# Performance work log

Hardware: AMD Instinct MI355X
Metric: run time of the kernel (lower is better)

The kernel has to match this reference:

```python
import jax, jax.numpy as jnp
import numpy as np

N_NODES = 100000
N_EDGES = 1600000
IN_D = 128
OUT_D = 128


def setup_inputs() -> dict:
    key = jax.random.key(0)
    ks = jax.random.split(key, 10)
    scale = 1.0 / np.sqrt(IN_D)
    inp = {
        "x": jax.random.normal(ks[0], (N_NODES, IN_D), dtype=jnp.float32),
        "edge_idx": jax.random.randint(ks[1], (2, N_EDGES), 0, N_NODES, dtype=jnp.int32),
        "W1": jax.random.normal(ks[2], (OUT_D, IN_D), dtype=jnp.float32) * scale,
        "b1": jax.random.normal(ks[3], (OUT_D,), dtype=jnp.float32) * scale,
        "W2": jax.random.normal(ks[4], (OUT_D, IN_D), dtype=jnp.float32) * scale,
        "b2": jax.random.normal(ks[5], (OUT_D,), dtype=jnp.float32) * scale,
        "W3": jax.random.normal(ks[6], (OUT_D, IN_D), dtype=jnp.float32) * scale,
        "b3": jax.random.normal(ks[7], (OUT_D,), dtype=jnp.float32) * scale,
        "W4": jax.random.normal(ks[8], (OUT_D, IN_D), dtype=jnp.float32) * scale,
        "b4": jax.random.normal(ks[9], (OUT_D,), dtype=jnp.float32) * scale,
    }
    return inp


def _message_passing(y, src, dst, num_nodes, add_self=True):
    # original: if add_self: x = x + x  (doubles features)
    if add_self:
        y = y + y
    # gather messages from source nodes, scatter-add into target nodes
    return jax.ops.segment_sum(y[src], dst, num_segments=num_nodes)


def reference(x, edge_idx, W1, b1, W2, b2, W3, b3, W4, b4):
    num_nodes = x.shape[0]
    src, dst = edge_idx[0], edge_idx[1]
    x1 = x @ W1.T + b1
    x2 = _message_passing(x @ W2.T + b2, src, dst, num_nodes)
    x3 = _message_passing(x @ W3.T + b3, src, dst, num_nodes)
    x4 = _message_passing(x @ W4.T + b4, src, dst, num_nodes)
    return jax.nn.sigmoid(x3 + x4) * x2 + x1
```

## Files before the change

kernel.cpp:

```cpp
#include <hip/hip_runtime.h>

__device__ __forceinline__ float bf2f(unsigned short u) {
    union { unsigned int i; float f; } v;
    v.i = ((unsigned int)u) << 16;
    return v.f;
}
__device__ __forceinline__ unsigned short f2bf(float f) {
    union { float f; unsigned int i; } v;
    v.f = f;
    unsigned int x = v.i;
    return (unsigned short)((x + 0x7fffu + ((x >> 16) & 1u)) >> 16);
}

typedef short bf16x8 __attribute__((ext_vector_type(8)));
typedef float f32x4 __attribute__((ext_vector_type(4)));

#define BSHIFT 9
#define BRANGE 512

__global__ void prep_kernel(const float* __restrict__ x,
                            const float* __restrict__ W1, const float* __restrict__ W2,
                            const float* __restrict__ W3, const float* __restrict__ W4,
                            unsigned short* __restrict__ xb, unsigned short* __restrict__ Wb,
                            int* __restrict__ deg, int* __restrict__ bcnt, int M, int nx4)
{
    int i = blockIdx.x * 256 + threadIdx.x;
    if (i < nx4) {
        float4 v = ((const float4*)x)[i];
        unsigned lo = (unsigned)f2bf(v.x) | ((unsigned)f2bf(v.y) << 16);
        unsigned hi = (unsigned)f2bf(v.z) | ((unsigned)f2bf(v.w) << 16);
        uint2 p; p.x = lo; p.y = hi;
        *(uint2*)(xb + (size_t)i * 4) = p;
    }
    if (deg && i < M) deg[i] = 0;
    if (bcnt && i < 256) bcnt[i] = 0;
    if (i < 16384) {
        Wb[i]         = f2bf(W1[i]);
        Wb[16384 + i] = f2bf(W2[i]);
        Wb[32768 + i] = f2bf(W3[i] + W4[i]);
    }
}

__global__ __launch_bounds__(512) void bucket_hist_kernel(
    const int* __restrict__ dst, int* __restrict__ bcnt, int ne, int nb)
{
    __shared__ int h[256];
    int t = threadIdx.x;
    if (t < 256) h[t] = 0;
    __syncthreads();
    for (int i = blockIdx.x * 512 + t; i < ne; i += gridDim.x * 512)
        atomicAdd(&h[dst[i] >> BSHIFT], 1);
    __syncthreads();
    if (t < nb) {
        int c = h[t];
        if (c) atomicAdd(&bcnt[t], c);
    }
}

__global__ __launch_bounds__(256) void bucket_scan_kernel(
    const int* __restrict__ bcnt, int* __restrict__ boff, int* __restrict__ gcur, int nb)
{
    __shared__ int sh[256];
    int t = threadIdx.x;
    int v = (t < nb) ? bcnt[t] : 0;
    sh[t] = v;
    __syncthreads();
    int acc = v;
    for (int off = 1; off < 256; off <<= 1) {
        int y = (t >= off) ? sh[t - off] : 0;
        __syncthreads();
        acc += y;
        sh[t] = acc;
        __syncthreads();
    }
    if (t < nb) {
        boff[t + 1] = acc;
        gcur[t] = acc - v;
    }
    if (t == 0) boff[0] = 0;
}

__global__ __launch_bounds__(512) void bucketize_kernel(
    const int* __restrict__ src, const int* __restrict__ dst,
    int* __restrict__ gcur, int2* __restrict__ bucketed, int ne, int chunk)
{
    __shared__ int cnt[256];
    __shared__ int sbase[256];
    const int t = threadIdx.x;
    const int e0 = blockIdx.x * chunk;
    const int e1 = (e0 + chunk < ne) ? e0 + chunk : ne;

    if (t < 256) cnt[t] = 0;
    __syncthreads();
    for (int e = e0 + t; e < e1; e += 512)
        atomicAdd(&cnt[dst[e] >> BSHIFT], 1);
    __syncthreads();
    if (t < 256) {
        int c = cnt[t];
        sbase[t] = c ? atomicAdd(&gcur[t], c) : 0;
        cnt[t] = 0;
    }
    __syncthreads();
    for (int e = e0 + t; e < e1; e += 512) {
        int d = dst[e];
        int b = d >> BSHIFT;
        int loc = atomicAdd(&cnt[b], 1);
        int2 v; v.x = src[e]; v.y = d;
        bucketed[sbase[b] + loc] = v;
    }
}

__global__ __launch_bounds__(512) void bucket_count_kernel(
    const int2* __restrict__ bucketed, const int* __restrict__ boff,
    int* __restrict__ deg, int M)
{
    __shared__ int cnt[BRANGE];
    const int t = threadIdx.x;
    const int b = blockIdx.x;
    cnt[t] = 0;
    __syncthreads();
    const int lo = boff[b], hi = boff[b + 1];
    for (int i = lo + t; i < hi; i += 512)
        atomicAdd(&cnt[bucketed[i].y & (BRANGE - 1)], 1);
    __syncthreads();
    int node = (b << BSHIFT) + t;
    if (node < M) deg[node] = cnt[t];
}

__global__ __launch_bounds__(512) void bucket_fill_kernel(
    const int2* __restrict__ bucketed, const int* __restrict__ boff,
    const int* __restrict__ offs, int* __restrict__ csr, int M)
{
    __shared__ int cur[BRANGE];
    const int t = threadIdx.x;
    const int b = blockIdx.x;
    int node = (b << BSHIFT) + t;
    cur[t] = (node < M) ? offs[node] : 0;
    __syncthreads();
    const int lo = boff[b], hi = boff[b + 1];
    for (int i = lo + t; i < hi; i += 512) {
        int2 e = bucketed[i];
        int p = atomicAdd(&cur[e.y & (BRANGE - 1)], 1);
        csr[p] = e.x;
    }
}

__global__ void hist_kernel(const int* __restrict__ dst, int* __restrict__ deg, int ne) {
    int e = blockIdx.x * blockDim.x + threadIdx.x;
    if (e < ne) atomicAdd(&deg[dst[e]], 1);
}

__global__ __launch_bounds__(1024) void scan_local_kernel(
    const int* __restrict__ deg, int* __restrict__ offs, int* __restrict__ bsum, int n)
{
    __shared__ int sh[1024];
    int t = threadIdx.x;
    int i = blockIdx.x * 1024 + t;
    int v = (i < n) ? deg[i] : 0;
    sh[t] = v;
    __syncthreads();
    int acc = v;
    for (int off = 1; off < 1024; off <<= 1) {
        int y = (t >= off) ? sh[t - off] : 0;
        __syncthreads();
        acc += y;
        sh[t] = acc;
        __syncthreads();
    }
    if (i < n) offs[i] = acc - v;
    if (t == 1023) bsum[blockIdx.x] = acc;
}

__global__ __launch_bounds__(128) void scan_totals_kernel(
    int* __restrict__ bsum, int* __restrict__ offs, int nb, int n)
{
    __shared__ int sh[128];
    int t = threadIdx.x;
    int v = (t < nb) ? bsum[t] : 0;
    sh[t] = v;
    __syncthreads();
    int acc = v;
    for (int off = 1; off < 128; off <<= 1) {
        int y = (t >= off) ? sh[t - off] : 0;
        __syncthreads();
        acc += y;
        sh[t] = acc;
        __syncthreads();
    }
    if (t < nb) bsum[t] = acc - v;
    if (t == 127) offs[n] = acc;
}

__global__ __launch_bounds__(1024) void scan_finalize_kernel(
    int* __restrict__ offs, const int* __restrict__ bsum, int* __restrict__ cursor, int n)
{
    int i = blockIdx.x * 1024 + threadIdx.x;
    if (i < n) {
        int o = offs[i] + bsum[i >> 10];
        offs[i] = o;
        if (cursor) cursor[i] = o;
    }
}

__global__ __launch_bounds__(256) void fill_csr_ranged_kernel(
    const int* __restrict__ src, const int* __restrict__ dst,
    int* __restrict__ cursor, int* __restrict__ csr, int ne, int rangeSize)
{
    const int r = blockIdx.x & 7;
    const int cb = blockIdx.x >> 3;
    const int nchunk = gridDim.x >> 3;
    const unsigned lo = (unsigned)(r * rangeSize);
    for (int e = cb * 256 + threadIdx.x; e < ne; e += nchunk * 256) {
        int d = dst[e];
        int s = src[e];
        if ((unsigned)(d - lo) < (unsigned)rangeSize) {
            int pos = atomicAdd(&cursor[d], 1);
            csr[pos] = s;
        }
    }
}

template<bool BF16SRC>
__global__ __launch_bounds__(256) void gather_kernel(
    const void* __restrict__ xsrc, const int* __restrict__ offs,
    const int* __restrict__ csr, unsigned short* __restrict__ gb, int M)
{
    const int wave = threadIdx.x >> 6;
    const int lane = threadIdx.x & 63;
    const int node = blockIdx.x * 4 + wave;
    if (node >= M) return;
    const int e0 = offs[node];
    const int e1 = offs[node + 1];

    float s0 = 0.f, s1 = 0.f, t0 = 0.f, t1 = 0.f;
    for (int e = e0; e < e1; e += 8) {
        int id[8];
        float m[8];
#pragma unroll
        for (int j = 0; j < 8; ++j) {
            int ee = e + j;
            bool ok = ee < e1;
            id[j] = csr[ok ? ee : e1 - 1];
            m[j] = ok ? 1.f : 0.f;
        }
#pragma unroll
        for (int j = 0; j < 8; ++j) {
            float lo, hi;
            if (BF16SRC) {
                unsigned v = *(const unsigned*)((const unsigned short*)xsrc +
                                                (size_t)id[j] * 128 + lane * 2);
                lo = bf2f((unsigned short)(v & 0xffffu));
                hi = bf2f((unsigned short)(v >> 16));
            } else {
                float2 v = *(const float2*)((const float*)xsrc +
                                            (size_t)id[j] * 128 + lane * 2);
                lo = v.x;
                hi = v.y;
            }
            if (j & 1) { t0 += m[j] * lo; t1 += m[j] * hi; }
            else       { s0 += m[j] * lo; s1 += m[j] * hi; }
        }
    }
    unsigned pk = (unsigned)f2bf(s0 + t0) | ((unsigned)f2bf(s1 + t1) << 16);
    *(unsigned*)(gb + (size_t)node * 128 + lane * 2) = pk;
}

template<bool XBF16>
__global__ __launch_bounds__(256) void gemm_kernel(
    const void* __restrict__ xsrc, const unsigned short* __restrict__ gb,
    const int* __restrict__ deg, const unsigned short* __restrict__ Wb,
    const float* __restrict__ B1, const float* __restrict__ B2,
    const float* __restrict__ B3, const float* __restrict__ B4,
    float* __restrict__ out, int M)
{
    __shared__ unsigned short x_lds[32 * 136];
    __shared__ unsigned short g_lds[32 * 136];

    const int t = threadIdx.x;
    const int wave = t >> 6;
    const int lane = t & 63;
    const int ln = lane & 15;
    const int quad = lane >> 4;
    const int row0 = blockIdx.x * 32;

    if (XBF16) {
        const unsigned short* xb = (const unsigned short*)xsrc;
#pragma unroll
        for (int i = 0; i < 2; ++i) {
            int c = i * 256 + t;
            int row = c >> 4;
            int koff = (c & 15) * 8;
            int grow = row0 + row;
            if (grow > M - 1) grow = M - 1;
            *(uint4*)&x_lds[row * 136 + koff] =
                *(const uint4*)(xb + (size_t)grow * 128 + koff);
        }
    } else {
        const float* xf = (const float*)xsrc;
#pragma unroll
        for (int i = 0; i < 4; ++i) {
            int c = i * 256 + t;
            int row = c >> 5;
            int koff = (c & 31) * 4;
            int grow = row0 + row;
            if (grow > M - 1) grow = M - 1;
            float4 v = *(const float4*)(xf + (size_t)grow * 128 + koff);
            unsigned p0 = (unsigned)f2bf(v.x) | ((unsigned)f2bf(v.y) << 16);
            unsigned p1 = (unsigned)f2bf(v.z) | ((unsigned)f2bf(v.w) << 16);
            *(unsigned*)&x_lds[row * 136 + koff]     = p0;
            *(unsigned*)&x_lds[row * 136 + koff + 2] = p1;
        }
    }
#pragma unroll
    for (int i = 0; i < 2; ++i) {
        int c = i * 256 + t;
        int row = c >> 4;
        int koff = (c & 15) * 8;
        int grow = row0 + row;
        if (grow > M - 1) grow = M - 1;
        *(uint4*)&g_lds[row * 136 + koff] =
            *(const uint4*)(gb + (size_t)grow * 128 + koff);
    }
    __syncthreads();

    f32x4 acc[3][2][2];
#pragma unroll
    for (int p = 0; p < 3; ++p)
#pragma unroll
        for (int rt = 0; rt < 2; ++rt)
#pragma unroll
            for (int c = 0; c < 2; ++c) {
                acc[p][rt][c][0] = 0.f; acc[p][rt][c][1] = 0.f;
                acc[p][rt][c][2] = 0.f; acc[p][rt][c][3] = 0.f;
            }

#pragma unroll
    for (int kk = 0; kk < 4; ++kk) {
        bf16x8 ax[2], ag[2];
#pragma unroll
        for (int rt = 0; rt < 2; ++rt) {
            ax[rt] = *(const bf16x8*)&x_lds[(rt * 16 + ln) * 136 + kk * 32 + quad * 8];
            ag[rt] = *(const bf16x8*)&g_lds[(rt * 16 + ln) * 136 + kk * 32 + quad * 8];
        }
#pragma unroll
        for (int p = 0; p < 3; ++p) {
#pragma unroll
            for (int c = 0; c < 2; ++c) {
                int col = wave * 32 + c * 16 + ln;
                bf16x8 bw = *(const bf16x8*)(Wb + (size_t)p * 16384 +
                                             (size_t)col * 128 + kk * 32 + quad * 8);
#pragma unroll
                for (int rt = 0; rt < 2; ++rt) {
                    acc[p][rt][c] = __builtin_amdgcn_mfma_f32_16x16x32_bf16(
                        (p == 0) ? ax[rt] : ag[rt], bw, acc[p][rt][c], 0, 0, 0);
                }
            }
        }
    }

#pragma unroll
    for (int rt = 0; rt < 2; ++rt) {
#pragma unroll
        for (int i = 0; i < 4; ++i) {
            int row = row0 + rt * 16 + quad * 4 + i;
            if (row < M) {
                float dg = (float)deg[row];
#pragma unroll
                for (int c = 0; c < 2; ++c) {
                    int col = wave * 32 + c * 16 + ln;
                    float p1 = acc[0][rt][c][i] + B1[col];
                    float h2 = 2.f * (acc[1][rt][c][i] + dg * B2[col]);
                    float z  = 2.f * (acc[2][rt][c][i] + dg * (B3[col] + B4[col]));
                    float g = 1.f / (1.f + __expf(-z));
                    out[(size_t)row * 128 + col] = g * h2 + p1;
                }
            }
        }
    }
}

extern "C" void kernel_launch(void* const* d_in, const int* in_sizes, int n_in,
                              void* d_out, int out_size, void* d_ws, size_t ws_size,
                              hipStream_t stream) {
    const float* x  = (const float*)d_in[0];
    const int* eidx = (const int*)d_in[1];
    const float* W1 = (const float*)d_in[2];
    const float* B1 = (const float*)d_in[3];
    const float* W2 = (const float*)d_in[4];
    const float* B2 = (const float*)d_in[5];
    const float* W3 = (const float*)d_in[6];
    const float* B3 = (const float*)d_in[7];
    const float* W4 = (const float*)d_in[8];
    const float* B4 = (const float*)d_in[9];
    float* out      = (float*)d_out;

    const int M  = in_sizes[0] / 128;
    const int NE = in_sizes[1] / 2;
    const int* src = eidx;
    const int* dst = eidx + NE;

    const int NB = (M + BRANGE - 1) >> BSHIFT;

    auto pad = [](size_t b) { return (b + 127) & ~(size_t)127; };
    const size_t xb_bytes  = pad((size_t)M * 128 * 2);
    const size_t gb_bytes  = pad((size_t)M * 128 * 2);
    const size_t wb_bytes  = pad((size_t)3 * 16384 * 2);
    const size_t deg_bytes = pad((size_t)M * 4);
    const size_t off_bytes = pad((size_t)(M + 1) * 4);
    const size_t csr_bytes = pad((size_t)NE * 4);
    const size_t bkt_bytes = pad((size_t)NE * 8);

    const size_t need_full = xb_bytes + gb_bytes + wb_bytes + deg_bytes + off_bytes +
                             1024 + csr_bytes + bkt_bytes + 4 * 1024;
    const bool full = (NB <= 256) && ws_size >= need_full + 1024;

    char* ws = (char*)d_ws;
    size_t off = 0;
    auto take = [&](size_t bytes) -> char* {
        char* p = ws + off;
        off = (off + bytes + 127) & ~(size_t)127;
        return p;
    };

    const int nbScan = (M + 1023) / 1024;

    if (full) {
        unsigned short* xb = (unsigned short*)take(xb_bytes);
        unsigned short* gb = (unsigned short*)take(gb_bytes);
        unsigned short* Wb = (unsigned short*)take(wb_bytes);
        int* deg   = (int*)take((size_t)M * 4);
        int* offs  = (int*)take((size_t)(M + 1) * 4);
        int* bsum  = (int*)take(256 * 4);
        int* csr   = (int*)take((size_t)NE * 4);
        int2* bkt  = (int2*)take((size_t)NE * 8);
        int* bcnt  = (int*)take(256 * 4);
        int* boff  = (int*)take(257 * 4);
        int* gcur  = (int*)take(256 * 4);

        const int nx4 = M * 128 / 4;
        const int chunk = (NE + 255) / 256;

        prep_kernel<<<(M * 32 + 255) / 256, 256, 0, stream>>>(
            x, W1, W2, W3, W4, xb, Wb, deg, bcnt, M, nx4);
        bucket_hist_kernel<<<256, 512, 0, stream>>>(dst, bcnt, NE, NB);
        bucket_scan_kernel<<<1, 256, 0, stream>>>(bcnt, boff, gcur, NB);
        bucketize_kernel<<<256, 512, 0, stream>>>(src, dst, gcur, bkt, NE, chunk);
        bucket_count_kernel<<<NB, 512, 0, stream>>>(bkt, boff, deg, M);
        scan_local_kernel<<<nbScan, 1024, 0, stream>>>(deg, offs, bsum, M);
        scan_totals_kernel<<<1, 128, 0, stream>>>(bsum, offs, nbScan, M);
        scan_finalize_kernel<<<nbScan, 1024, 0, stream>>>(offs, bsum, nullptr, M);
        bucket_fill_kernel<<<NB, 512, 0, stream>>>(bkt, boff, offs, csr, M);
        gather_kernel<true><<<(M + 3) / 4, 256, 0, stream>>>(xb, offs, csr, gb, M);
        gemm_kernel<true><<<(M + 31) / 32, 256, 0, stream>>>(
            xb, gb, deg, Wb, B1, B2, B3, B4, out, M);
    } else {
        unsigned short* gb = (unsigned short*)take(gb_bytes);
        unsigned short* Wb = (unsigned short*)take(wb_bytes);
        int* deg    = (int*)take((size_t)M * 4);
        int* offs   = (int*)take((size_t)(M + 1) * 4);
        int* cursor = (int*)take((size_t)M * 4);
        int* bsum   = (int*)take(256 * 4);
        int* csr    = (int*)take((size_t)NE * 4);

        const int prep_elems = (M > 16384 ? M : 16384);
        const int rangeSize = (M + 7) / 8;
        prep_kernel<<<(prep_elems + 255) / 256, 256, 0, stream>>>(
            x, W1, W2, W3, W4, nullptr, Wb, deg, nullptr, M, 0);
        hist_kernel<<<(NE + 255) / 256, 256, 0, stream>>>(dst, deg, NE);
        scan_local_kernel<<<nbScan, 1024, 0, stream>>>(deg, offs, bsum, M);
        scan_totals_kernel<<<1, 128, 0, stream>>>(bsum, offs, nbScan, M);
        scan_finalize_kernel<<<nbScan, 1024, 0, stream>>>(offs, bsum, cursor, M);
        fill_csr_ranged_kernel<<<2048, 256, 0, stream>>>(src, dst, cursor, csr, NE, rangeSize);
        gather_kernel<false><<<(M + 3) / 4, 256, 0, stream>>>(x, offs, csr, gb, M);
        gemm_kernel<false><<<(M + 31) / 32, 256, 0, stream>>>(
            x, gb, deg, Wb, B1, B2, B3, B4, out, M);
    }
}
```

Measured before the change: 289.1 us.

## Fuse bucket histogram into prep and merge CSR count/scan/fill kernels

The coarse bucket histogram now runs inside the bf16 conversion kernel on its first 256 blocks. Each block writes a per-block partial row, so the global atomics and the zeroing pass are no longer needed. The per-bucket count, global scan and fill kernels are replaced by a single bucket_finalize kernel. It counts degrees, does a 512-wide local scan offset by the bucket start to produce CSR offsets, then scatters sources. This removes several kernel launches and passes over the bucketed edge array, at the cost of a serial 256-row reduction in the scan kernel and uneven work in the histogram blocks.

```diff
diff --git a/kernel.cpp b/kernel.cpp
--- a/kernel.cpp
+++ b/kernel.cpp
@@ -18,11 +18,147 @@
 #define BSHIFT 9
 #define BRANGE 512
 
+__global__ __launch_bounds__(256) void prep_hist_kernel(
+    const float* __restrict__ x,
+    const float* __restrict__ W1, const float* __restrict__ W2,
+    const float* __restrict__ W3, const float* __restrict__ W4,
+    unsigned short* __restrict__ xb, unsigned short* __restrict__ Wb,
+    const int* __restrict__ dst, int* __restrict__ bpart,
+    int M, int nx4, int ne)
+{
+    __shared__ int h[256];
+    const int t = threadIdx.x;
+    const int blk = blockIdx.x;
+    const bool histBlock = (blk < 256);
+    if (histBlock) {
+        h[t] = 0;
+        __syncthreads();
+    }
+
+    int i = blk * 256 + t;
+    if (i < nx4) {
+        float4 v = ((const float4*)x)[i];
+        unsigned lo = (unsigned)f2bf(v.x) | ((unsigned)f2bf(v.y) << 16);
+        unsigned hi = (unsigned)f2bf(v.z) | ((unsigned)f2bf(v.w) << 16);
+        uint2 p; p.x = lo; p.y = hi;
+        *(uint2*)(xb + (size_t)i * 4) = p;
+    }
+    if (i < 16384) {
+        Wb[i]         = f2bf(W1[i]);
+        Wb[16384 + i] = f2bf(W2[i]);
+        Wb[32768 + i] = f2bf(W3[i] + W4[i]);
+    }
+
+    if (histBlock) {
+        for (int e = blk * 256 + t; e < ne; e += 65536)
+            atomicAdd(&h[dst[e] >> BSHIFT], 1);
+        __syncthreads();
+        bpart[blk * 256 + t] = h[t];
+    }
+}
+
+__global__ __launch_bounds__(256) void bucket_scan_kernel(
+    const int* __restrict__ bpart, int* __restrict__ boff, int* __restrict__ gcur, int nb)
+{
+    __shared__ int sh[256];
+    int t = threadIdx.x;
+    int v = 0;
+    for (int k = 0; k < 256; ++k) v += bpart[k * 256 + t];
+    if (t >= nb) v = 0;
+    sh[t] = v;
+    __syncthreads();
+    int acc = v;
+    for (int off = 1; off < 256; off <<= 1) {
+        int y = (t >= off) ? sh[t - off] : 0;
+        __syncthreads();
+        acc += y;
+        sh[t] = acc;
+        __syncthreads();
+    }
+    if (t < nb) {
+        boff[t + 1] = acc;
+        gcur[t] = acc - v;
+    }
+    if (t == 0) boff[0] = 0;
+}
+
+__global__ __launch_bounds__(512) void bucketize_kernel(
+    const int* __restrict__ src, const int* __restrict__ dst,
+    int* __restrict__ gcur, int2* __restrict__ bucketed, int ne, int chunk)
+{
+    __shared__ int cnt[256];
+    __shared__ int sbase[256];
+    const int t = threadIdx.x;
+    const int e0 = blockIdx.x * chunk;
+    const int e1 = (e0 + chunk < ne) ? e0 + chunk : ne;
+
+    if (t < 256) cnt[t] = 0;
+    __syncthreads();
+    for (int e = e0 + t; e < e1; e += 512)
+        atomicAdd(&cnt[dst[e] >> BSHIFT], 1);
+    __syncthreads();
+    if (t < 256) {
+        int c = cnt[t];
+        sbase[t] = c ? atomicAdd(&gcur[t], c) : 0;
+        cnt[t] = 0;
+    }
+    __syncthreads();
+    for (int e = e0 + t; e < e1; e += 512) {
+        int d = dst[e];
+        int b = d >> BSHIFT;
+        int loc = atomicAdd(&cnt[b], 1);
+        int2 v; v.x = src[e]; v.y = d;
+        bucketed[sbase[b] + loc] = v;
+    }
+}
+
+__global__ __launch_bounds__(512) void bucket_finalize_kernel(
+    const int2* __restrict__ bucketed, const int* __restrict__ boff,
+    int* __restrict__ offs, int* __restrict__ deg, int* __restrict__ csr,
+    int M, int nb)
+{
+    __shared__ int cnt[BRANGE];
+    __shared__ int sc[BRANGE];
+    const int t = threadIdx.x;
+    const int b = blockIdx.x;
+    cnt[t] = 0;
+    __syncthreads();
+    const int lo = boff[b], hi = boff[b + 1];
+    for (int i = lo + t; i < hi; i += 512)
+        atomicAdd(&cnt[bucketed[i].y & (BRANGE - 1)], 1);
+    __syncthreads();
+    const int v = cnt[t];
+    sc[t] = v;
+    __syncthreads();
+    int acc = v;
+    for (int off = 1; off < 512; off <<= 1) {
+        int y = (t >= off) ? sc[t - off] : 0;
+        __syncthreads();
+        acc += y;
+        sc[t] = acc;
+        __syncthreads();
+    }
+    const int excl = acc - v;
+    const int node = (b << BSHIFT) + t;
+    if (node < M) {
+        offs[node] = lo + excl;
+        deg[node] = v;
+    }
+    if (b == nb - 1 && t == 0) offs[M] = hi;
+    cnt[t] = lo + excl;
+    __syncthreads();
+    for (int i = lo + t; i < hi; i += 512) {
+        int2 e = bucketed[i];
+        int p = atomicAdd(&cnt[e.y & (BRANGE - 1)], 1);
+        csr[p] = e.x;
+    }
+}
+
 __global__ void prep_kernel(const float* __restrict__ x,
                             const float* __restrict__ W1, const float* __restrict__ W2,
                             const float* __restrict__ W3, const float* __restrict__ W4,
                             unsigned short* __restrict__ xb, unsigned short* __restrict__ Wb,
-                            int* __restrict__ deg, int* __restrict__ bcnt, int M, int nx4)
+                            int* __restrict__ deg, int M, int nx4)
 {
     int i = blockIdx.x * 256 + threadIdx.x;
     if (i < nx4) {
@@ -33,115 +169,10 @@
         *(uint2*)(xb + (size_t)i * 4) = p;
     }
     if (deg && i < M) deg[i] = 0;
-    if (bcnt && i < 256) bcnt[i] = 0;
     if (i < 16384) {
         Wb[i]         = f2bf(W1[i]);
         Wb[16384 + i] = f2bf(W2[i]);
         Wb[32768 + i] = f2bf(W3[i] + W4[i]);
-    }
-}
-
-__global__ __launch_bounds__(512) void bucket_hist_kernel(
-    const int* __restrict__ dst, int* __restrict__ bcnt, int ne, int nb)
-{
-    __shared__ int h[256];
-    int t = threadIdx.x;
-    if (t < 256) h[t] = 0;
-    __syncthreads();
-    for (int i = blockIdx.x * 512 + t; i < ne; i += gridDim.x * 512)
-        atomicAdd(&h[dst[i] >> BSHIFT], 1);
-    __syncthreads();
-    if (t < nb) {
-        int c = h[t];
-        if (c) atomicAdd(&bcnt[t], c);
-    }
-}
-
-__global__ __launch_bounds__(256) void bucket_scan_kernel(
-    const int* __restrict__ bcnt, int* __restrict__ boff, int* __restrict__ gcur, int nb)
-{
-    __shared__ int sh[256];
-    int t = threadIdx.x;
-    int v = (t < nb) ? bcnt[t] : 0;
-    sh[t] = v;
-    __syncthreads();
-    int acc = v;
-    for (int off = 1; off < 256; off <<= 1) {
-        int y = (t >= off) ? sh[t - off] : 0;
-        __syncthreads();
-        acc += y;
-        sh[t] = acc;
-        __syncthreads();
-    }
-    if (t < nb) {
-        boff[t + 1] = acc;
-        gcur[t] = acc - v;
-    }
-    if (t == 0) boff[0] = 0;
-}
-
-__global__ __launch_bounds__(512) void bucketize_kernel(
-    const int* __restrict__ src, const int* __restrict__ dst,
-    int* __restrict__ gcur, int2* __restrict__ bucketed, int ne, int chunk)
-{
-    __shared__ int cnt[256];
-    __shared__ int sbase[256];
-    const int t = threadIdx.x;
-    const int e0 = blockIdx.x * chunk;
-    const int e1 = (e0 + chunk < ne) ? e0 + chunk : ne;
-
-    if (t < 256) cnt[t] = 0;
-    __syncthreads();
-    for (int e = e0 + t; e < e1; e += 512)
-        atomicAdd(&cnt[dst[e] >> BSHIFT], 1);
-    __syncthreads();
-    if (t < 256) {
-        int c = cnt[t];
-        sbase[t] = c ? atomicAdd(&gcur[t], c) : 0;
-        cnt[t] = 0;
-    }
-    __syncthreads();
-    for (int e = e0 + t; e < e1; e += 512) {
-        int d = dst[e];
-        int b = d >> BSHIFT;
-        int loc = atomicAdd(&cnt[b], 1);
-        int2 v; v.x = src[e]; v.y = d;
-        bucketed[sbase[b] + loc] = v;
-    }
-}
-
-__global__ __launch_bounds__(512) void bucket_count_kernel(
-    const int2* __restrict__ bucketed, const int* __restrict__ boff,
-    int* __restrict__ deg, int M)
-{
-    __shared__ int cnt[BRANGE];
-    const int t = threadIdx.x;
-    const int b = blockIdx.x;
-    cnt[t] = 0;
-    __syncthreads();
-    const int lo = boff[b], hi = boff[b + 1];
-    for (int i = lo + t; i < hi; i += 512)
-        atomicAdd(&cnt[bucketed[i].y & (BRANGE - 1)], 1);
-    __syncthreads();
-    int node = (b << BSHIFT) + t;
-    if (node < M) deg[node] = cnt[t];
-}
-
-__global__ __launch_bounds__(512) void bucket_fill_kernel(
-    const int2* __restrict__ bucketed, const int* __restrict__ boff,
-    const int* __restrict__ offs, int* __restrict__ csr, int M)
-{
-    __shared__ int cur[BRANGE];
-    const int t = threadIdx.x;
-    const int b = blockIdx.x;
-    int node = (b << BSHIFT) + t;
-    cur[t] = (node < M) ? offs[node] : 0;
-    __syncthreads();
-    const int lo = boff[b], hi = boff[b + 1];
-    for (int i = lo + t; i < hi; i += 512) {
-        int2 e = bucketed[i];
-        int p = atomicAdd(&cur[e.y & (BRANGE - 1)], 1);
-        csr[p] = e.x;
     }
 }
 
@@ -409,9 +440,10 @@
     const size_t off_bytes = pad((size_t)(M + 1) * 4);
     const size_t csr_bytes = pad((size_t)NE * 4);
     const size_t bkt_bytes = pad((size_t)NE * 8);
+    const size_t bpart_bytes = pad((size_t)256 * 256 * 4);
 
     const size_t need_full = xb_bytes + gb_bytes + wb_bytes + deg_bytes + off_bytes +
-                             1024 + csr_bytes + bkt_bytes + 4 * 1024;
+                             csr_bytes + bkt_bytes + bpart_bytes + 4 * 1024;
     const bool full = (NB <= 256) && ws_size >= need_full + 1024;
 
     char* ws = (char*)d_ws;
@@ -428,28 +460,24 @@
         unsigned short* xb = (unsigned short*)take(xb_bytes);
         unsigned short* gb = (unsigned short*)take(gb_bytes);
         unsigned short* Wb = (unsigned short*)take(wb_bytes);
-        int* deg   = (int*)take((size_t)M * 4);
-        int* offs  = (int*)take((size_t)(M + 1) * 4);
-        int* bsum  = (int*)take(256 * 4);
-        int* csr   = (int*)take((size_t)NE * 4);
-        int2* bkt  = (int2*)take((size_t)NE * 8);
-        int* bcnt  = (int*)take(256 * 4);
-        int* boff  = (int*)take(257 * 4);
-        int* gcur  = (int*)take(256 * 4);
+        int* deg    = (int*)take((size_t)M * 4);
+        int* offs   = (int*)take((size_t)(M + 1) * 4);
+        int* csr    = (int*)take((size_t)NE * 4);
+        int2* bkt   = (int2*)take((size_t)NE * 8);
+        int* bpart  = (int*)take((size_t)256 * 256 * 4);
+        int* boff   = (int*)take(257 * 4);
+        int* gcur   = (int*)take(256 * 4);
 
         const int nx4 = M * 128 / 4;
         const int chunk = (NE + 255) / 256;
-
-        prep_kernel<<<(M * 32 + 255) / 256, 256, 0, stream>>>(
-            x, W1, W2, W3, W4, xb, Wb, deg, bcnt, M, nx4);
-        bucket_hist_kernel<<<256, 512, 0, stream>>>(dst, bcnt, NE, NB);
-        bucket_scan_kernel<<<1, 256, 0, stream>>>(bcnt, boff, gcur, NB);
+        int prep_grid = (M * 32 + 255) / 256;
+        if (prep_grid < 256) prep_grid = 256;
+
+        prep_hist_kernel<<<prep_grid, 256, 0, stream>>>(
+            x, W1, W2, W3, W4, xb, Wb, dst, bpart, M, nx4, NE);
+        bucket_scan_kernel<<<1, 256, 0, stream>>>(bpart, boff, gcur, NB);
         bucketize_kernel<<<256, 512, 0, stream>>>(src, dst, gcur, bkt, NE, chunk);
-        bucket_count_kernel<<<NB, 512, 0, stream>>>(bkt, boff, deg, M);
-        scan_local_kernel<<<nbScan, 1024, 0, stream>>>(deg, offs, bsum, M);
-        scan_totals_kernel<<<1, 128, 0, stream>>>(bsum, offs, nbScan, M);
-        scan_finalize_kernel<<<nbScan, 1024, 0, stream>>>(offs, bsum, nullptr, M);
-        bucket_fill_kernel<<<NB, 512, 0, stream>>>(bkt, boff, offs, csr, M);
+        bucket_finalize_kernel<<<NB, 512, 0, stream>>>(bkt, boff, offs, deg, csr, M, NB);
         gather_kernel<true><<<(M + 3) / 4, 256, 0, stream>>>(xb, offs, csr, gb, M);
         gemm_kernel<true><<<(M + 31) / 32, 256, 0, stream>>>(
             xb, gb, deg, Wb, B1, B2, B3, B4, out, M);
@@ -465,7 +493,7 @@
         const int prep_elems = (M > 16384 ? M : 16384);
         const int rangeSize = (M + 7) / 8;
         prep_kernel<<<(prep_elems + 255) / 256, 256, 0, stream>>>(
-            x, W1, W2, W3, W4, nullptr, Wb, deg, nullptr, M, 0);
+            x, W1, W2, W3, W4, nullptr, Wb, deg, M, 0);
         hist_kernel<<<(NE + 255) / 256, 256, 0, stream>>>(dst, deg, NE);
         scan_local_kernel<<<nbScan, 1024, 0, stream>>>(deg, offs, bsum, M);
         scan_totals_kernel<<<1, 128, 0, stream>>>(bsum, offs, nbScan, M);
```

Measured after the change: 282.1 us. 1.02x faster.
